# Optimization experiments

Hardware: AMD Instinct MI355X
Metric: run time of the kernel (lower is better)

## Reference

```python
import jax, jax.numpy as jnp
import numpy as np

B, T, C = 4, 2048, 1024
H = 16
D = C // H  # head_size = 64


def setup_inputs() -> dict:
    key = jax.random.key(0)
    k1, k2, k3 = jax.random.split(key, 3)
    x = jax.random.normal(k1, (B, T, C), dtype=jnp.float32)
    # weights stored pre-transposed relative to torch nn.Linear: y = x @ w
    w_attn = jax.random.normal(k2, (C, 3 * C), dtype=jnp.float32) * (1.0 / np.sqrt(C))
    w_proj = jax.random.normal(k3, (C, C), dtype=jnp.float32) * (1.0 / np.sqrt(C))
    return {"x": x, "w_attn": w_attn, "w_proj": w_proj}


def reference(x, w_attn, w_proj):
    # Dropout layers are identity in eval mode (reference baseline).
    Bx, Tx, Cx = x.shape
    qkv = x @ w_attn                                   # [B,T,3C]
    q, k, v = jnp.split(qkv, 3, axis=2)
    # [B,T,C] -> [B,H,T,D]
    def heads(t):
        return t.reshape(Bx, Tx, H, D).transpose(0, 2, 1, 3)
    q, k, v = heads(q), heads(k), heads(v)
    scale = 1.0 / np.sqrt(D).astype(np.float32)
    att = jnp.einsum('bhqd,bhkd->bhqk', q, k) * scale   # [B,H,T,T]
    causal = jnp.tril(jnp.ones((Tx, Tx), dtype=bool))
    att = jnp.where(causal[None, None], att, -jnp.inf)
    att = jax.nn.softmax(att, axis=-1)
    y = jnp.einsum('bhqk,bhkd->bhqd', att, v)           # [B,H,T,D]
    y = y.transpose(0, 2, 1, 3).reshape(Bx, Tx, Cx)     # [B,T,C]
    return y @ w_proj
```

## Files before the change

kernel.cpp:

```cpp
#include <hip/hip_runtime.h>

typedef unsigned short ushort;
typedef short short8 __attribute__((ext_vector_type(8)));
typedef float f32x4 __attribute__((ext_vector_type(4)));
typedef __attribute__((address_space(3))) unsigned int lds_u32;
typedef __attribute__((address_space(1))) const unsigned int glb_u32;

#define DEVI static __device__ __forceinline__

DEVI ushort f2b(float f) {
  union { float f; unsigned u; } x; x.f = f;
  unsigned r = x.u + 0x7fffu + ((x.u >> 16) & 1u);
  return (ushort)(r >> 16);
}

DEVI void gload_lds16(const ushort* g, ushort* l) {
  __builtin_amdgcn_global_load_lds((glb_u32*)g, (lds_u32*)l, 16, 0, 0);
}

__global__ void cast_bf16_kernel(const float* __restrict__ in, ushort* __restrict__ out, int n8) {
  int i = blockIdx.x * blockDim.x + threadIdx.x;
  if (i >= n8) return;
  const float4* p = (const float4*)in + 2 * (size_t)i;
  float4 a = p[0], b = p[1];
  ushort tmp[8] = { f2b(a.x), f2b(a.y), f2b(a.z), f2b(a.w),
                    f2b(b.x), f2b(b.y), f2b(b.z), f2b(b.w) };
  *(short8*)(out + 8 * (size_t)i) = *(short8*)tmp;
}

__global__ void transpose_cast_kernel(const float* __restrict__ in, ushort* __restrict__ out,
                                      int R, int C) {
  __shared__ float tile[32][33];
  int bx = blockIdx.x * 32, by = blockIdx.y * 32;
  int tx = threadIdx.x, ty = threadIdx.y;
#pragma unroll
  for (int i = 0; i < 32; i += 8)
    tile[ty + i][tx] = in[(size_t)(by + ty + i) * C + bx + tx];
  __syncthreads();
#pragma unroll
  for (int i = 0; i < 32; i += 8)
    out[(size_t)(bx + ty + i) * R + by + tx] = f2b(tile[tx][ty + i]);
}

__global__ __launch_bounds__(256) void transpose_v_kernel(const ushort* __restrict__ qkv,
                                                          ushort* __restrict__ vt) {
  __shared__ ushort t[64][66];
  const int tile = blockIdx.x;
  const int bh = blockIdx.y;
  const int b = bh >> 4, h = bh & 15;
  const int tx = threadIdx.x & 31, ty = threadIdx.x >> 5;
  const uint* src = (const uint*)(qkv + (size_t)(b * 2048 + tile * 64) * 3072 + 2048 + h * 64);
#pragma unroll
  for (int i = 0; i < 64; i += 8)
    *(uint*)&t[ty + i][tx * 2] = src[(size_t)(ty + i) * 1536 + tx];
  __syncthreads();
  uint* dst = (uint*)(vt + (size_t)bh * 64 * 2048);
#pragma unroll
  for (int i = 0; i < 64; i += 8) {
    int d = ty + i;
    uint lo = t[tx * 2][d], hi = t[tx * 2 + 1][d];
    dst[(size_t)d * 1024 + tile * 32 + tx] = lo | (hi << 16);
  }
}

template <bool OUT_F32>
__global__ __launch_bounds__(256) void gemm_bt_kernel(
    const ushort* __restrict__ A, const ushort* __restrict__ BT,
    void* __restrict__ C_, int M, int N, int K) {
  __shared__ ushort lA[128 * 32];
  __shared__ ushort lB[128 * 32];
  const int tid = threadIdx.x, lane = tid & 63, wave = tid >> 6;
  const int wr = wave >> 1, wc = wave & 1;
  const int m0 = blockIdx.x * 128, n0 = blockIdx.y * 128;
  const int g = lane >> 4, c = lane & 15;
  f32x4 acc[4][4] = {};
  for (int kt = 0; kt < K; kt += 32) {
    __syncthreads();
#pragma unroll
    for (int it = 0; it < 2; ++it) {
      int idx = it * 256 + tid;
      int row = idx >> 2, ch = idx & 3;
      gload_lds16(A + (size_t)(m0 + row) * K + kt + ch * 8,
                  lA + (size_t)(it * 256 + wave * 64) * 8);
      gload_lds16(BT + (size_t)(n0 + row) * K + kt + ch * 8,
                  lB + (size_t)(it * 256 + wave * 64) * 8);
    }
    __syncthreads();
    short8 af[4], bf[4];
#pragma unroll
    for (int mi = 0; mi < 4; ++mi)
      af[mi] = *(const short8*)&lA[(wr * 64 + mi * 16 + c) * 32 + g * 8];
#pragma unroll
    for (int ni = 0; ni < 4; ++ni)
      bf[ni] = *(const short8*)&lB[(wc * 64 + ni * 16 + c) * 32 + g * 8];
#pragma unroll
    for (int mi = 0; mi < 4; ++mi)
#pragma unroll
      for (int ni = 0; ni < 4; ++ni)
        acc[mi][ni] = __builtin_amdgcn_mfma_f32_16x16x32_bf16(af[mi], bf[ni], acc[mi][ni], 0, 0, 0);
  }
#pragma unroll
  for (int mi = 0; mi < 4; ++mi)
#pragma unroll
    for (int ni = 0; ni < 4; ++ni)
#pragma unroll
      for (int r = 0; r < 4; ++r) {
        int mrow = m0 + wr * 64 + mi * 16 + g * 4 + r;
        int ncol = n0 + wc * 64 + ni * 16 + c;
        if (OUT_F32) ((float*)C_)[(size_t)mrow * N + ncol] = acc[mi][ni][r];
        else         ((ushort*)C_)[(size_t)mrow * N + ncol] = f2b(acc[mi][ni][r]);
      }
}

DEVI void attn_compute(const short8 (&qf)[2], f32x4 (&o)[4], float (&l)[4],
                       int qb_t, int kv, const ushort* __restrict__ kb,
                       const ushort* __restrict__ vb, ushort* __restrict__ pW,
                       int wave, int g, int c, int e) {
  const float C1 = 0.18033688011112042f;
  const float SH = 17.312340490667562f;
  f32x4 s[4];
#pragma unroll
  for (int n = 0; n < 4; ++n) {
    short8 kf0 = *(const short8*)&kb[(n * 16 + c) * 64 + ((g ^ e) * 8)];
    short8 kf1 = *(const short8*)&kb[(n * 16 + c) * 64 + (((4 + g) ^ e) * 8)];
    s[n] = (f32x4){0.f, 0.f, 0.f, 0.f};
    s[n] = __builtin_amdgcn_mfma_f32_16x16x32_bf16(qf[0], kf0, s[n], 0, 0, 0);
    s[n] = __builtin_amdgcn_mfma_f32_16x16x32_bf16(qf[1], kf1, s[n], 0, 0, 0);
  }
  if (kv == qb_t) {
#pragma unroll
    for (int n = 0; n < 4; ++n)
#pragma unroll
      for (int r = 0; r < 4; ++r)
        if ((n * 16 + c) > (wave * 16 + g * 4 + r)) s[n][r] = -INFINITY;
  }
#pragma unroll
  for (int n = 0; n < 4; ++n)
#pragma unroll
    for (int r = 0; r < 4; ++r) {
      float p = __builtin_amdgcn_exp2f(fmaf(s[n][r], C1, -SH));
      l[r] += p;
      union { float f; unsigned u; } pu; pu.f = p;
      int row = g * 4 + r;
      pW[row * 64 + (((n * 2 + (c >> 3)) ^ (row & 7)) * 8) + (c & 7)] =
          (ushort)((pu.u + 0x8000u) >> 16);
    }
  short8 pf0 = *(const short8*)&pW[c * 64 + ((g ^ e) * 8)];
  short8 pf1 = *(const short8*)&pW[c * 64 + (((4 + g) ^ e) * 8)];
#pragma unroll
  for (int dg = 0; dg < 4; ++dg) {
    short8 vf0 = *(const short8*)&vb[(dg * 16 + c) * 64 + ((g ^ e) * 8)];
    short8 vf1 = *(const short8*)&vb[(dg * 16 + c) * 64 + (((4 + g) ^ e) * 8)];
    o[dg] = __builtin_amdgcn_mfma_f32_16x16x32_bf16(pf0, vf0, o[dg], 0, 0, 0);
    o[dg] = __builtin_amdgcn_mfma_f32_16x16x32_bf16(pf1, vf1, o[dg], 0, 0, 0);
  }
}

DEVI void attn_store(const f32x4 (&o)[4], float (&l)[4], ushort* __restrict__ y,
                     int b, int h, int qb_t, int wave, int g, int c) {
#pragma unroll
  for (int r = 0; r < 4; ++r) {
    float s0 = l[r];
    s0 += __shfl_xor(s0, 1);
    s0 += __shfl_xor(s0, 2);
    s0 += __shfl_xor(s0, 4);
    s0 += __shfl_xor(s0, 8);
    l[r] = 1.0f / s0;
  }
#pragma unroll
  for (int dg = 0; dg < 4; ++dg)
#pragma unroll
    for (int r = 0; r < 4; ++r) {
      size_t row = (size_t)b * 2048 + qb_t * 64 + wave * 16 + g * 4 + r;
      y[row * 1024 + h * 64 + dg * 16 + c] = f2b(o[dg][r] * l[r]);
    }
}

__global__ __launch_bounds__(256, 2) void attn_kernel(
    const ushort* __restrict__ qkv, const ushort* __restrict__ vt,
    ushort* __restrict__ y) {
  __shared__ ushort kT[2][64 * 64];
  __shared__ ushort vT[2][64 * 64];
  __shared__ ushort pB[4][16 * 64];
  const int tid = threadIdx.x, lane = tid & 63, wave = tid >> 6;
  const int g = lane >> 4, c = lane & 15, e = c & 7;
  const int j = blockIdx.x, bh = blockIdx.y;
  const int b = bh >> 4, h = bh & 15;
  const int qb0 = j, qb1 = 31 - j;
  const size_t base = (size_t)b * 2048 * 3072 + (size_t)h * 64;
  const ushort* qp = qkv + base;
  const ushort* kp = qkv + base + 1024;
  const ushort* vp = vt + (size_t)bh * 64 * 2048;

  short8 qf0[2], qf1[2];
  {
    int qrow0 = qb0 * 64 + wave * 16 + c;
    int qrow1 = qb1 * 64 + wave * 16 + c;
    qf0[0] = *(const short8*)(qp + (size_t)qrow0 * 3072 + g * 8);
    qf0[1] = *(const short8*)(qp + (size_t)qrow0 * 3072 + 32 + g * 8);
    qf1[0] = *(const short8*)(qp + (size_t)qrow1 * 3072 + g * 8);
    qf1[1] = *(const short8*)(qp + (size_t)qrow1 * 3072 + 32 + g * 8);
  }
  f32x4 o0[4] = {}, o1[4] = {};
  float l0[4] = {0.f, 0.f, 0.f, 0.f}, l1[4] = {0.f, 0.f, 0.f, 0.f};

  auto stage = [&](int kv, int buf) {
#pragma unroll
    for (int it = 0; it < 2; ++it) {
      int idx = it * 256 + tid;
      int row = idx >> 3, ch = idx & 7;
      int chs = ch ^ (row & 7);
      gload_lds16(kp + (size_t)(kv * 64 + row) * 3072 + chs * 8, kT[buf] + idx * 8);
      gload_lds16(vp + (size_t)row * 2048 + kv * 64 + chs * 8, vT[buf] + idx * 8);
    }
  };

  stage(0, 0);
  __syncthreads();
  int cur = 0;
  for (int kv = 0; kv <= qb1; ++kv) {
    if (kv < qb1) stage(kv + 1, cur ^ 1);
    attn_compute(qf1, o1, l1, qb1, kv, kT[cur], vT[cur], pB[wave], wave, g, c, e);
    if (kv <= qb0)
      attn_compute(qf0, o0, l0, qb0, kv, kT[cur], vT[cur], pB[wave], wave, g, c, e);
    __syncthreads();
    cur ^= 1;
  }

  attn_store(o0, l0, y, b, h, qb0, wave, g, c);
  attn_store(o1, l1, y, b, h, qb1, wave, g, c);
}

extern "C" void kernel_launch(void* const* d_in, const int* in_sizes, int n_in,
                              void* d_out, int out_size, void* d_ws, size_t ws_size,
                              hipStream_t stream) {
  const float* x      = (const float*)d_in[0];
  const float* w_attn = (const float*)d_in[1];
  const float* w_proj = (const float*)d_in[2];
  float* out = (float*)d_out;

  ushort* xb   = (ushort*)d_ws;
  ushort* watT = xb   + (size_t)8192 * 1024;
  ushort* wpT  = watT + (size_t)3072 * 1024;
  ushort* qkvb = wpT  + (size_t)1024 * 1024;
  ushort* yb   = qkvb + (size_t)8192 * 3072;
  ushort* vtb  = yb   + (size_t)8192 * 1024;

  cast_bf16_kernel<<<4096, 256, 0, stream>>>(x, xb, 8192 * 1024 / 8);
  transpose_cast_kernel<<<dim3(96, 32), dim3(32, 8), 0, stream>>>(w_attn, watT, 1024, 3072);
  transpose_cast_kernel<<<dim3(32, 32), dim3(32, 8), 0, stream>>>(w_proj, wpT, 1024, 1024);

  gemm_bt_kernel<false><<<dim3(64, 24), 256, 0, stream>>>(xb, watT, qkvb, 8192, 3072, 1024);
  transpose_v_kernel<<<dim3(32, 64), 256, 0, stream>>>(qkvb, vtb);
  attn_kernel<<<dim3(16, 64), 256, 0, stream>>>(qkvb, vtb, yb);
  gemm_bt_kernel<true><<<dim3(64, 8), 256, 0, stream>>>(yb, wpT, out, 8192, 1024, 1024);
}
```

Measured before the change: 203.1 us.

## Double-buffer GEMM with 256x128 tiles, swizzled LDS, and XCD-aware block remap

Rewrites the bf16 GEMM kernel to use 512-thread blocks computing 256x128 output tiles with a K-step of 64. It double-buffers the LDS tiles so global-to-LDS loads for the next step overlap MFMA work on the current one. An XOR swizzle on the LDS layout is meant to avoid bank conflicts. Block indices are remapped in groups of 8 for cache locality across dies, and s_setprio is raised around the MFMA bursts. The larger tiles use more LDS (about 96KB), which halves the block count and may reduce occupancy.

After: 215.8 us. +6.3%, slower.

```diff
diff --git a/kernel.cpp b/kernel.cpp
--- a/kernel.cpp
+++ b/kernel.cpp
@@ -64,40 +64,71 @@
 }
 
 template <bool OUT_F32>
-__global__ __launch_bounds__(256) void gemm_bt_kernel(
+__global__ __launch_bounds__(512) void gemm256_kernel(
     const ushort* __restrict__ A, const ushort* __restrict__ BT,
     void* __restrict__ C_, int M, int N, int K) {
-  __shared__ ushort lA[128 * 32];
-  __shared__ ushort lB[128 * 32];
+  __shared__ ushort lA[2][256 * 64];
+  __shared__ ushort lB[2][128 * 64];
   const int tid = threadIdx.x, lane = tid & 63, wave = tid >> 6;
   const int wr = wave >> 1, wc = wave & 1;
-  const int m0 = blockIdx.x * 128, n0 = blockIdx.y * 128;
   const int g = lane >> 4, c = lane & 15;
+  const int nx = gridDim.x;
+  const int nwg = nx * gridDim.y;
+  int lin = blockIdx.y * nx + blockIdx.x;
+  lin = (lin & 7) * (nwg >> 3) + (lin >> 3);
+  const int m0 = (lin % nx) * 256, n0 = (lin / nx) * 128;
+
+  auto stageA = [&](int kt, int buf) {
+#pragma unroll
+    for (int it = 0; it < 4; ++it) {
+      int idx = it * 512 + tid;
+      int row = idx >> 3, ch = idx & 7;
+      int chs = ch ^ (row & 7);
+      gload_lds16(A + (size_t)(m0 + row) * K + kt + chs * 8, lA[buf] + idx * 8);
+    }
+  };
+  auto stageB = [&](int kt, int buf) {
+#pragma unroll
+    for (int it = 0; it < 2; ++it) {
+      int idx = it * 512 + tid;
+      int row = idx >> 3, ch = idx & 7;
+      int chs = ch ^ (row & 7);
+      gload_lds16(BT + (size_t)(n0 + row) * K + kt + chs * 8, lB[buf] + idx * 8);
+    }
+  };
+
   f32x4 acc[4][4] = {};
-  for (int kt = 0; kt < K; kt += 32) {
+  stageA(0, 0);
+  stageB(0, 0);
+  __syncthreads();
+  const int nt = K >> 6;
+  for (int t = 0; t < nt; ++t) {
+    const int cur = t & 1;
+    if (t + 1 < nt) { stageA((t + 1) << 6, cur ^ 1); stageB((t + 1) << 6, cur ^ 1); }
+    const ushort* a_ = lA[cur];
+    const ushort* b_ = lB[cur];
+    short8 bf[4][2];
+#pragma unroll
+    for (int ni = 0; ni < 4; ++ni) {
+      int rb = wc * 64 + ni * 16 + c;
+#pragma unroll
+      for (int kk = 0; kk < 2; ++kk)
+        bf[ni][kk] = *(const short8*)&b_[rb * 64 + (((kk * 4 + g) ^ (rb & 7)) * 8)];
+    }
+#pragma unroll
+    for (int mi = 0; mi < 4; ++mi) {
+      int ra = wr * 64 + mi * 16 + c;
+      short8 af0 = *(const short8*)&a_[ra * 64 + ((g ^ (ra & 7)) * 8)];
+      short8 af1 = *(const short8*)&a_[ra * 64 + (((4 + g) ^ (ra & 7)) * 8)];
+      __builtin_amdgcn_s_setprio(1);
+#pragma unroll
+      for (int ni = 0; ni < 4; ++ni) {
+        acc[mi][ni] = __builtin_amdgcn_mfma_f32_16x16x32_bf16(af0, bf[ni][0], acc[mi][ni], 0, 0, 0);
+        acc[mi][ni] = __builtin_amdgcn_mfma_f32_16x16x32_bf16(af1, bf[ni][1], acc[mi][ni], 0, 0, 0);
+      }
+      __builtin_amdgcn_s_setprio(0);
+    }
     __syncthreads();
-#pragma unroll
-    for (int it = 0; it < 2; ++it) {
-      int idx = it * 256 + tid;
-      int row = idx >> 2, ch = idx & 3;
-      gload_lds16(A + (size_t)(m0 + row) * K + kt + ch * 8,
-                  lA + (size_t)(it * 256 + wave * 64) * 8);
-      gload_lds16(BT + (size_t)(n0 + row) * K + kt + ch * 8,
-                  lB + (size_t)(it * 256 + wave * 64) * 8);
-    }
-    __syncthreads();
-    short8 af[4], bf[4];
-#pragma unroll
-    for (int mi = 0; mi < 4; ++mi)
-      af[mi] = *(const short8*)&lA[(wr * 64 + mi * 16 + c) * 32 + g * 8];
-#pragma unroll
-    for (int ni = 0; ni < 4; ++ni)
-      bf[ni] = *(const short8*)&lB[(wc * 64 + ni * 16 + c) * 32 + g * 8];
-#pragma unroll
-    for (int mi = 0; mi < 4; ++mi)
-#pragma unroll
-      for (int ni = 0; ni < 4; ++ni)
-        acc[mi][ni] = __builtin_amdgcn_mfma_f32_16x16x32_bf16(af[mi], bf[ni], acc[mi][ni], 0, 0, 0);
   }
 #pragma unroll
   for (int mi = 0; mi < 4; ++mi)
@@ -250,8 +281,8 @@
   transpose_cast_kernel<<<dim3(96, 32), dim3(32, 8), 0, stream>>>(w_attn, watT, 1024, 3072);
   transpose_cast_kernel<<<dim3(32, 32), dim3(32, 8), 0, stream>>>(w_proj, wpT, 1024, 1024);
 
-  gemm_bt_kernel<false><<<dim3(64, 24), 256, 0, stream>>>(xb, watT, qkvb, 8192, 3072, 1024);
+  gemm256_kernel<false><<<dim3(32, 24), 512, 0, stream>>>(xb, watT, qkvb, 8192, 3072, 1024);
   transpose_v_kernel<<<dim3(32, 64), 256, 0, stream>>>(qkvb, vtb);
   attn_kernel<<<dim3(16, 64), 256, 0, stream>>>(qkvb, vtb, yb);
-  gemm_bt_kernel<true><<<dim3(64, 8), 256, 0, stream>>>(yb, wpT, out, 8192, 1024, 1024);
-}
+  gemm256_kernel<true><<<dim3(32, 8), 512, 0, stream>>>(yb, wpT, out, 8192, 1024, 1024);
+}
```

## Use 32x32x16 MFMA and split query blocks across wave pairs in attention

Applied to the files above, without the earlier changes.

The attention kernel moves from 16x16x32 MFMA tiles, where each wave handled 16 rows of both paired query blocks, to 32x32x16 MFMA tiles. Each pair of waves now owns one of the two query blocks, and each wave covers 32 query rows. This is meant to cut K/V LDS fragment reloads per flop and use the larger MFMA shape. The cost is load imbalance: the wave pair holding the shorter query block idles for many kv iterations while still hitting the barrier. It also doubles the P scratch buffer in LDS.

New measurement: 233.9 us. 1.15x slower.

```diff
diff --git a/kernel.cpp b/kernel.cpp
--- a/kernel.cpp
+++ b/kernel.cpp
@@ -3,6 +3,7 @@
 typedef unsigned short ushort;
 typedef short short8 __attribute__((ext_vector_type(8)));
 typedef float f32x4 __attribute__((ext_vector_type(4)));
+typedef float f32x16 __attribute__((ext_vector_type(16)));
 typedef __attribute__((address_space(3))) unsigned int lds_u32;
 typedef __attribute__((address_space(1))) const unsigned int glb_u32;
 
@@ -112,97 +113,38 @@
       }
 }
 
-DEVI void attn_compute(const short8 (&qf)[2], f32x4 (&o)[4], float (&l)[4],
-                       int qb_t, int kv, const ushort* __restrict__ kb,
-                       const ushort* __restrict__ vb, ushort* __restrict__ pW,
-                       int wave, int g, int c, int e) {
-  const float C1 = 0.18033688011112042f;
-  const float SH = 17.312340490667562f;
-  f32x4 s[4];
-#pragma unroll
-  for (int n = 0; n < 4; ++n) {
-    short8 kf0 = *(const short8*)&kb[(n * 16 + c) * 64 + ((g ^ e) * 8)];
-    short8 kf1 = *(const short8*)&kb[(n * 16 + c) * 64 + (((4 + g) ^ e) * 8)];
-    s[n] = (f32x4){0.f, 0.f, 0.f, 0.f};
-    s[n] = __builtin_amdgcn_mfma_f32_16x16x32_bf16(qf[0], kf0, s[n], 0, 0, 0);
-    s[n] = __builtin_amdgcn_mfma_f32_16x16x32_bf16(qf[1], kf1, s[n], 0, 0, 0);
-  }
-  if (kv == qb_t) {
-#pragma unroll
-    for (int n = 0; n < 4; ++n)
-#pragma unroll
-      for (int r = 0; r < 4; ++r)
-        if ((n * 16 + c) > (wave * 16 + g * 4 + r)) s[n][r] = -INFINITY;
-  }
-#pragma unroll
-  for (int n = 0; n < 4; ++n)
-#pragma unroll
-    for (int r = 0; r < 4; ++r) {
-      float p = __builtin_amdgcn_exp2f(fmaf(s[n][r], C1, -SH));
-      l[r] += p;
-      union { float f; unsigned u; } pu; pu.f = p;
-      int row = g * 4 + r;
-      pW[row * 64 + (((n * 2 + (c >> 3)) ^ (row & 7)) * 8) + (c & 7)] =
-          (ushort)((pu.u + 0x8000u) >> 16);
-    }
-  short8 pf0 = *(const short8*)&pW[c * 64 + ((g ^ e) * 8)];
-  short8 pf1 = *(const short8*)&pW[c * 64 + (((4 + g) ^ e) * 8)];
-#pragma unroll
-  for (int dg = 0; dg < 4; ++dg) {
-    short8 vf0 = *(const short8*)&vb[(dg * 16 + c) * 64 + ((g ^ e) * 8)];
-    short8 vf1 = *(const short8*)&vb[(dg * 16 + c) * 64 + (((4 + g) ^ e) * 8)];
-    o[dg] = __builtin_amdgcn_mfma_f32_16x16x32_bf16(pf0, vf0, o[dg], 0, 0, 0);
-    o[dg] = __builtin_amdgcn_mfma_f32_16x16x32_bf16(pf1, vf1, o[dg], 0, 0, 0);
-  }
-}
-
-DEVI void attn_store(const f32x4 (&o)[4], float (&l)[4], ushort* __restrict__ y,
-                     int b, int h, int qb_t, int wave, int g, int c) {
-#pragma unroll
-  for (int r = 0; r < 4; ++r) {
-    float s0 = l[r];
-    s0 += __shfl_xor(s0, 1);
-    s0 += __shfl_xor(s0, 2);
-    s0 += __shfl_xor(s0, 4);
-    s0 += __shfl_xor(s0, 8);
-    l[r] = 1.0f / s0;
-  }
-#pragma unroll
-  for (int dg = 0; dg < 4; ++dg)
-#pragma unroll
-    for (int r = 0; r < 4; ++r) {
-      size_t row = (size_t)b * 2048 + qb_t * 64 + wave * 16 + g * 4 + r;
-      y[row * 1024 + h * 64 + dg * 16 + c] = f2b(o[dg][r] * l[r]);
-    }
-}
-
 __global__ __launch_bounds__(256, 2) void attn_kernel(
     const ushort* __restrict__ qkv, const ushort* __restrict__ vt,
     ushort* __restrict__ y) {
   __shared__ ushort kT[2][64 * 64];
   __shared__ ushort vT[2][64 * 64];
-  __shared__ ushort pB[4][16 * 64];
+  __shared__ ushort pB[4][32 * 64];
   const int tid = threadIdx.x, lane = tid & 63, wave = tid >> 6;
-  const int g = lane >> 4, c = lane & 15, e = c & 7;
+  const int col = lane & 31, hi = lane >> 5;
   const int j = blockIdx.x, bh = blockIdx.y;
   const int b = bh >> 4, h = bh & 15;
   const int qb0 = j, qb1 = 31 - j;
+  const int wpair = wave >> 1, whalf = wave & 1;
+  const int qb_t = wpair ? qb1 : qb0;
   const size_t base = (size_t)b * 2048 * 3072 + (size_t)h * 64;
   const ushort* qp = qkv + base;
   const ushort* kp = qkv + base + 1024;
   const ushort* vp = vt + (size_t)bh * 64 * 2048;
 
-  short8 qf0[2], qf1[2];
+  const float C1 = 0.18033688011112042f;
+  const float SH = 17.312340490667562f;
+
+  short8 qa[4];
   {
-    int qrow0 = qb0 * 64 + wave * 16 + c;
-    int qrow1 = qb1 * 64 + wave * 16 + c;
-    qf0[0] = *(const short8*)(qp + (size_t)qrow0 * 3072 + g * 8);
-    qf0[1] = *(const short8*)(qp + (size_t)qrow0 * 3072 + 32 + g * 8);
-    qf1[0] = *(const short8*)(qp + (size_t)qrow1 * 3072 + g * 8);
-    qf1[1] = *(const short8*)(qp + (size_t)qrow1 * 3072 + 32 + g * 8);
-  }
-  f32x4 o0[4] = {}, o1[4] = {};
-  float l0[4] = {0.f, 0.f, 0.f, 0.f}, l1[4] = {0.f, 0.f, 0.f, 0.f};
+    int qrow = qb_t * 64 + whalf * 32 + col;
+#pragma unroll
+    for (int ks = 0; ks < 4; ++ks)
+      qa[ks] = *(const short8*)(qp + (size_t)qrow * 3072 + ks * 16 + hi * 8);
+  }
+  f32x16 o0 = (f32x16)(0.0f), o1 = (f32x16)(0.0f);
+  float lr[16];
+#pragma unroll
+  for (int r = 0; r < 16; ++r) lr[r] = 0.f;
 
   auto stage = [&](int kv, int buf) {
 #pragma unroll
@@ -220,15 +162,66 @@
   int cur = 0;
   for (int kv = 0; kv <= qb1; ++kv) {
     if (kv < qb1) stage(kv + 1, cur ^ 1);
-    attn_compute(qf1, o1, l1, qb1, kv, kT[cur], vT[cur], pB[wave], wave, g, c, e);
-    if (kv <= qb0)
-      attn_compute(qf0, o0, l0, qb0, kv, kT[cur], vT[cur], pB[wave], wave, g, c, e);
+    if (kv <= qb_t) {
+      const ushort* kb = kT[cur];
+      const ushort* vb = vT[cur];
+      ushort* pW = pB[wave];
+      f32x16 s0 = (f32x16)(0.0f), s1 = (f32x16)(0.0f);
+      const int kr1 = 32 + col;
+#pragma unroll
+      for (int ks = 0; ks < 4; ++ks) {
+        short8 kf0 = *(const short8*)&kb[col * 64 + (((ks * 2 + hi) ^ (col & 7)) * 8)];
+        short8 kf1 = *(const short8*)&kb[kr1 * 64 + (((ks * 2 + hi) ^ (kr1 & 7)) * 8)];
+        s0 = __builtin_amdgcn_mfma_f32_32x32x16_bf16(qa[ks], kf0, s0, 0, 0, 0);
+        s1 = __builtin_amdgcn_mfma_f32_32x32x16_bf16(qa[ks], kf1, s1, 0, 0, 0);
+      }
+      const bool diag = (kv == qb_t);
+#pragma unroll
+      for (int r = 0; r < 16; ++r) {
+        int rowl = (r & 3) + 8 * (r >> 2) + 4 * hi;
+        int qloc = whalf * 32 + rowl;
+        float sv0 = s0[r], sv1 = s1[r];
+        if (diag && col > qloc) sv0 = -INFINITY;
+        if (diag && 32 + col > qloc) sv1 = -INFINITY;
+        float p0 = __builtin_amdgcn_exp2f(fmaf(sv0, C1, -SH));
+        float p1 = __builtin_amdgcn_exp2f(fmaf(sv1, C1, -SH));
+        lr[r] += p0 + p1;
+        union { float f; unsigned u; } u0, u1;
+        u0.f = p0; u1.f = p1;
+        int sb = rowl * 64 + (col & 7);
+        int c0 = (col >> 3) ^ (rowl & 7);
+        int c1 = ((32 + col) >> 3) ^ (rowl & 7);
+        pW[sb + c0 * 8] = (ushort)((u0.u + 0x8000u) >> 16);
+        pW[sb + c1 * 8] = (ushort)((u1.u + 0x8000u) >> 16);
+      }
+      const int vr1 = 32 + col;
+#pragma unroll
+      for (int ks = 0; ks < 4; ++ks) {
+        short8 pf  = *(const short8*)&pW[col * 64 + (((ks * 2 + hi) ^ (col & 7)) * 8)];
+        short8 vf0 = *(const short8*)&vb[col * 64 + (((ks * 2 + hi) ^ (col & 7)) * 8)];
+        short8 vf1 = *(const short8*)&vb[vr1 * 64 + (((ks * 2 + hi) ^ (vr1 & 7)) * 8)];
+        o0 = __builtin_amdgcn_mfma_f32_32x32x16_bf16(pf, vf0, o0, 0, 0, 0);
+        o1 = __builtin_amdgcn_mfma_f32_32x32x16_bf16(pf, vf1, o1, 0, 0, 0);
+      }
+    }
     __syncthreads();
     cur ^= 1;
   }
 
-  attn_store(o0, l0, y, b, h, qb0, wave, g, c);
-  attn_store(o1, l1, y, b, h, qb1, wave, g, c);
+#pragma unroll
+  for (int r = 0; r < 16; ++r) {
+    float s0 = lr[r];
+    s0 += __shfl_xor(s0, 1);
+    s0 += __shfl_xor(s0, 2);
+    s0 += __shfl_xor(s0, 4);
+    s0 += __shfl_xor(s0, 8);
+    s0 += __shfl_xor(s0, 16);
+    float inv = 1.0f / s0;
+    int rowl = (r & 3) + 8 * (r >> 2) + 4 * hi;
+    size_t row = (size_t)b * 2048 + qb_t * 64 + whalf * 32 + rowl;
+    y[row * 1024 + h * 64 + col]      = f2b(o0[r] * inv);
+    y[row * 1024 + h * 64 + 32 + col] = f2b(o1[r] * inv);
+  }
 }
 
 extern "C" void kernel_launch(void* const* d_in, const int* in_sizes, int n_in,
```

## Merge prep casts into one kernel and split attention into one q-block per workgroup

Applied to the files above, without the earlier changes.

The x cast and both weight transpose-casts move into a single prep kernel that picks its work by block index, which saves two launches. The attention kernel stops pairing q-blocks j and 31-j in one workgroup and instead launches 32×64 workgroups that each handle one q-block, with the longest blocks scheduled first via reversed indexing. This doubles the parallelism and halves register state per workgroup, but loses the load balance the pairing gave and the sharing of K/V tile loads between the two q-blocks.

Result: slower. 229.1 us (+12.8%).

```diff
diff --git a/kernel.cpp b/kernel.cpp
--- a/kernel.cpp
+++ b/kernel.cpp
@@ -18,21 +18,30 @@
   __builtin_amdgcn_global_load_lds((glb_u32*)g, (lds_u32*)l, 16, 0, 0);
 }
 
-__global__ void cast_bf16_kernel(const float* __restrict__ in, ushort* __restrict__ out, int n8) {
-  int i = blockIdx.x * blockDim.x + threadIdx.x;
-  if (i >= n8) return;
-  const float4* p = (const float4*)in + 2 * (size_t)i;
-  float4 a = p[0], b = p[1];
-  ushort tmp[8] = { f2b(a.x), f2b(a.y), f2b(a.z), f2b(a.w),
-                    f2b(b.x), f2b(b.y), f2b(b.z), f2b(b.w) };
-  *(short8*)(out + 8 * (size_t)i) = *(short8*)tmp;
-}
-
-__global__ void transpose_cast_kernel(const float* __restrict__ in, ushort* __restrict__ out,
-                                      int R, int C) {
+__global__ __launch_bounds__(256) void prep_kernel(
+    const float* __restrict__ x, const float* __restrict__ wa,
+    const float* __restrict__ wp, ushort* __restrict__ xb,
+    ushort* __restrict__ watT, ushort* __restrict__ wpT) {
   __shared__ float tile[32][33];
-  int bx = blockIdx.x * 32, by = blockIdx.y * 32;
-  int tx = threadIdx.x, ty = threadIdx.y;
+  const int bid = blockIdx.x, tid = threadIdx.x;
+  if (bid < 4096) {
+    int i = bid * 256 + tid;
+    const float4* p = (const float4*)x + 2 * (size_t)i;
+    float4 a = p[0], b = p[1];
+    ushort tmp[8] = { f2b(a.x), f2b(a.y), f2b(a.z), f2b(a.w),
+                      f2b(b.x), f2b(b.y), f2b(b.z), f2b(b.w) };
+    *(short8*)(xb + 8 * (size_t)i) = *(short8*)tmp;
+    return;
+  }
+  const float* in; ushort* out; int R, C, bx, by;
+  if (bid < 7168) {
+    int bb = bid - 4096; in = wa; out = watT; R = 1024; C = 3072;
+    bx = (bb % 96) * 32; by = (bb / 96) * 32;
+  } else {
+    int bb = bid - 7168; in = wp; out = wpT; R = 1024; C = 1024;
+    bx = (bb % 32) * 32; by = (bb / 32) * 32;
+  }
+  const int tx = tid & 31, ty = tid >> 5;
 #pragma unroll
   for (int i = 0; i < 32; i += 8)
     tile[ty + i][tx] = in[(size_t)(by + ty + i) * C + bx + tx];
@@ -184,25 +193,21 @@
   __shared__ ushort pB[4][16 * 64];
   const int tid = threadIdx.x, lane = tid & 63, wave = tid >> 6;
   const int g = lane >> 4, c = lane & 15, e = c & 7;
-  const int j = blockIdx.x, bh = blockIdx.y;
+  const int jj = 31 - blockIdx.x, bh = blockIdx.y;
   const int b = bh >> 4, h = bh & 15;
-  const int qb0 = j, qb1 = 31 - j;
   const size_t base = (size_t)b * 2048 * 3072 + (size_t)h * 64;
   const ushort* qp = qkv + base;
   const ushort* kp = qkv + base + 1024;
   const ushort* vp = vt + (size_t)bh * 64 * 2048;
 
-  short8 qf0[2], qf1[2];
+  short8 qf[2];
   {
-    int qrow0 = qb0 * 64 + wave * 16 + c;
-    int qrow1 = qb1 * 64 + wave * 16 + c;
-    qf0[0] = *(const short8*)(qp + (size_t)qrow0 * 3072 + g * 8);
-    qf0[1] = *(const short8*)(qp + (size_t)qrow0 * 3072 + 32 + g * 8);
-    qf1[0] = *(const short8*)(qp + (size_t)qrow1 * 3072 + g * 8);
-    qf1[1] = *(const short8*)(qp + (size_t)qrow1 * 3072 + 32 + g * 8);
-  }
-  f32x4 o0[4] = {}, o1[4] = {};
-  float l0[4] = {0.f, 0.f, 0.f, 0.f}, l1[4] = {0.f, 0.f, 0.f, 0.f};
+    int qrow = jj * 64 + wave * 16 + c;
+    qf[0] = *(const short8*)(qp + (size_t)qrow * 3072 + g * 8);
+    qf[1] = *(const short8*)(qp + (size_t)qrow * 3072 + 32 + g * 8);
+  }
+  f32x4 o[4] = {};
+  float l[4] = {0.f, 0.f, 0.f, 0.f};
 
   auto stage = [&](int kv, int buf) {
 #pragma unroll
@@ -218,17 +223,14 @@
   stage(0, 0);
   __syncthreads();
   int cur = 0;
-  for (int kv = 0; kv <= qb1; ++kv) {
-    if (kv < qb1) stage(kv + 1, cur ^ 1);
-    attn_compute(qf1, o1, l1, qb1, kv, kT[cur], vT[cur], pB[wave], wave, g, c, e);
-    if (kv <= qb0)
-      attn_compute(qf0, o0, l0, qb0, kv, kT[cur], vT[cur], pB[wave], wave, g, c, e);
+  for (int kv = 0; kv <= jj; ++kv) {
+    if (kv < jj) stage(kv + 1, cur ^ 1);
+    attn_compute(qf, o, l, jj, kv, kT[cur], vT[cur], pB[wave], wave, g, c, e);
     __syncthreads();
     cur ^= 1;
   }
 
-  attn_store(o0, l0, y, b, h, qb0, wave, g, c);
-  attn_store(o1, l1, y, b, h, qb1, wave, g, c);
+  attn_store(o, l, y, b, h, jj, wave, g, c);
 }
 
 extern "C" void kernel_launch(void* const* d_in, const int* in_sizes, int n_in,
@@ -246,12 +248,9 @@
   ushort* yb   = qkvb + (size_t)8192 * 3072;
   ushort* vtb  = yb   + (size_t)8192 * 1024;
 
-  cast_bf16_kernel<<<4096, 256, 0, stream>>>(x, xb, 8192 * 1024 / 8);
-  transpose_cast_kernel<<<dim3(96, 32), dim3(32, 8), 0, stream>>>(w_attn, watT, 1024, 3072);
-  transpose_cast_kernel<<<dim3(32, 32), dim3(32, 8), 0, stream>>>(w_proj, wpT, 1024, 1024);
-
+  prep_kernel<<<8192, 256, 0, stream>>>(x, w_attn, w_proj, xb, watT, wpT);
   gemm_bt_kernel<false><<<dim3(64, 24), 256, 0, stream>>>(xb, watT, qkvb, 8192, 3072, 1024);
   transpose_v_kernel<<<dim3(32, 64), 256, 0, stream>>>(qkvb, vtb);
-  attn_kernel<<<dim3(16, 64), 256, 0, stream>>>(qkvb, vtb, yb);
+  attn_kernel<<<dim3(32, 64), 256, 0, stream>>>(qkvb, vtb, yb);
   gemm_bt_kernel<true><<<dim3(64, 8), 256, 0, stream>>>(yb, wpT, out, 8192, 1024, 1024);
 }
```
